# Kernel tuning notes

Hardware: AMD Instinct MI355X
Metric: run time of the kernel (lower is better)

The kernel has to match this reference:

```python
import jax, jax.numpy as jnp
import numpy as np

BITS = 50

def _xor(a, b):
    # binary XOR on {0,1} floats: a + b - 2ab
    return a + b - 2.0 * a * b

def _maj(a, b, c):
    # majority (carry-out of a full adder) on {0,1} floats
    return a * b + a * c + b * c - 2.0 * a * b * c

def setup_inputs() -> dict:
    key = jax.random.key(0)
    kA, kB = jax.random.split(key)
    N = 1_000_000
    A = jax.random.randint(kA, (N, BITS), 0, 2).astype(jnp.float32)
    B = jax.random.randint(kB, (N, BITS), 0, 2).astype(jnp.float32)
    return {"A": A, "B": B}

def reference(A, B):
    """A - B via two's complement ripple-carry: A + NOT(B) + 1, LSB first.
    Returns (result [..., 50], borrow [..., 1])."""
    not_b = 1.0 - B                      # VecNOT
    # scan over the 50 bits (sequential carry dependency)
    a_bits = jnp.moveaxis(A, -1, 0)      # [50, N]
    b_bits = jnp.moveaxis(not_b, -1, 0)  # [50, N]
    c0 = jnp.ones(A.shape[:-1], dtype=A.dtype)  # initial carry = 1

    def step(c, ab):
        a, b = ab
        s = _xor(_xor(a, b), c)          # FullAdder sum
        c_next = _maj(a, b, c)           # FullAdder carry
        return c_next, s

    c_final, sums = jax.lax.scan(step, c0, (a_bits, b_bits))
    result = jnp.moveaxis(sums, 0, -1)   # [N, 50]
    borrow = (1.0 - c_final)[..., None]  # borrow_not(carry), [N, 1]
    return result, borrow
```

## Files before the change

kernel.cpp:

```cpp
#include <hip/hip_runtime.h>


constexpr int BITS = 50;
constexpr unsigned long long MASK50 = (1ULL << BITS) - 1ULL;

__device__ inline unsigned long long shfl64(unsigned long long v, int src) {
    int lo = __shfl((int)(unsigned)(v & 0xffffffffULL), src, 64);
    int hi = __shfl((int)(unsigned)(v >> 32), src, 64);
    return ((unsigned long long)(unsigned)hi << 32) | (unsigned long long)(unsigned)lo;
}

__device__ inline unsigned long long spread2(unsigned long long x) {
    x = (x | (x << 16)) & 0x0000FFFF0000FFFFULL;
    x = (x | (x << 8))  & 0x00FF00FF00FF00FFULL;
    x = (x | (x << 4))  & 0x0F0F0F0F0F0F0F0FULL;
    x = (x | (x << 2))  & 0x3333333333333333ULL;
    x = (x | (x << 1))  & 0x5555555555555555ULL;
    return x;
}

__global__ __launch_bounds__(256) void Subtractor50Bit_kernel(
    const float* __restrict__ A, const float* __restrict__ B,
    float* __restrict__ out, int N)
{
    const int lane = threadIdx.x & 63;
    const int wv   = threadIdx.x >> 6;
    const long long waveIdx = (long long)blockIdx.x * 4 + wv;
    const long long rowBase = waveIdx * 64;
    if (rowBase >= N) return;

    if (rowBase + 64 <= N) {
        const long long eBase = rowBase * BITS;
        const float2* pa = (const float2*)(A + eBase) + lane;
        const float2* pb = (const float2*)(B + eBase) + lane;

        float2 fa[25], fb[25];
        #pragma unroll
        for (int t = 0; t < 25; ++t) fa[t] = pa[t * 64];
        #pragma unroll
        for (int t = 0; t < 25; ++t) fb[t] = pb[t * 64];

        __builtin_amdgcn_sched_barrier(0);

        unsigned long long wa = 0, wb = 0;
        const int  lane31 = lane & 31;
        const bool isLo   = lane < 32;
        #pragma unroll
        for (int t = 0; t < 25; ++t) {
            unsigned long long aE = __ballot(fa[t].x != 0.0f);
            unsigned long long aO = __ballot(fa[t].y != 0.0f);
            unsigned long long bE = __ballot(fb[t].x != 0.0f);
            unsigned long long bO = __ballot(fb[t].y != 0.0f);
            if (lane31 == t) {
                wa = isLo ? aE : aO;
                wb = isLo ? bE : bO;
            }
        }

        const int p0 = 25 * lane;
        const int w0 = p0 >> 6;
        const int sh = p0 & 63;

        unsigned long long aE0 = shfl64(wa, w0);
        unsigned long long aE1 = shfl64(wa, w0 + 1);
        unsigned long long aO0 = shfl64(wa, 32 + w0);
        unsigned long long aO1 = shfl64(wa, 33 + w0);
        unsigned long long bE0 = shfl64(wb, w0);
        unsigned long long bE1 = shfl64(wb, w0 + 1);
        unsigned long long bO0 = shfl64(wb, 32 + w0);
        unsigned long long bO1 = shfl64(wb, 33 + w0);

        unsigned long long evA = aE0 >> sh, odA = aO0 >> sh;
        unsigned long long evB = bE0 >> sh, odB = bO0 >> sh;
        if (sh > 39) {
            const int c = 64 - sh;
            evA |= aE1 << c; odA |= aO1 << c;
            evB |= bE1 << c; odB |= bO1 << c;
        }
        const unsigned long long M25 = (1ULL << 25) - 1ULL;
        evA &= M25; odA &= M25; evB &= M25; odB &= M25;

        unsigned long long av = spread2(evA) | (spread2(odA) << 1);
        unsigned long long bv = spread2(evB) | (spread2(odB) << 1);

        unsigned long long diff = (av - bv) & MASK50;
        float borrow = (av < bv) ? 1.0f : 0.0f;

        unsigned long long* po = (unsigned long long*)(out + eBase);
        #pragma unroll
        for (int j = 0; j < 25; ++j) {
            int q = j * 64 + lane;
            int r = q / 25;
            int k = 2 * (q - r * 25);
            unsigned long long dr = shfl64(diff, r);
            unsigned long long t2 = dr >> k;
            po[q] = ((t2 & 1ULL) ? 0x000000003F800000ULL : 0ULL)
                  | ((t2 & 2ULL) ? 0x3F80000000000000ULL : 0ULL);
        }
        out[(long long)N * BITS + rowBase + lane] = borrow;
    } else {
        long long r = rowBase + lane;
        if (r < N) {
            unsigned long long av = 0, bv = 0;
            for (int k = 0; k < BITS; ++k) {
                av |= (unsigned long long)(A[r * BITS + k] != 0.0f) << k;
                bv |= (unsigned long long)(B[r * BITS + k] != 0.0f) << k;
            }
            unsigned long long diff = (av - bv) & MASK50;
            for (int k = 0; k < BITS; ++k)
                out[r * BITS + k] = (float)((diff >> k) & 1ULL);
            out[(long long)N * BITS + r] = (av < bv) ? 1.0f : 0.0f;
        }
    }
}

extern "C" void kernel_launch(void* const* d_in, const int* in_sizes, int n_in,
                              void* d_out, int out_size, void* d_ws, size_t ws_size,
                              hipStream_t stream) {
    const float* A = (const float*)d_in[0];
    const float* B = (const float*)d_in[1];
    float* out = (float*)d_out;
    const int N = in_sizes[0] / BITS;

    const int waves  = (N + 63) / 64;
    const int blocks = (waves + 3) / 4;
    Subtractor50Bit_kernel<<<blocks, 256, 0, stream>>>(A, B, out, N);
}
```

Measured before the change: 447.8 us.

## Switch to grid-stride persistent waves and interleave loads with ballots

Replaces the one-wave-per-64-row-tile launch with a grid capped at 2048 blocks whose waves loop over tiles in grid-stride fashion, and adds an occupancy hint to launch bounds. The upfront loading of all 50 float2 values into registers, separated by a schedule barrier, is replaced by loading each pair inside the ballot loop. This cuts register pressure and block-launch overhead, but risks less memory-level parallelism per wave because loads are no longer all issued before the ballots. The tail rows are now handled by a single wave of block 0.

New measurement: 522.1 us. 16.6% more time.

```diff
diff --git a/kernel.cpp b/kernel.cpp
--- a/kernel.cpp
+++ b/kernel.cpp
@@ -19,38 +19,34 @@
     return x;
 }
 
-__global__ __launch_bounds__(256) void Subtractor50Bit_kernel(
+__global__ __launch_bounds__(256, 8) void Subtractor50Bit_kernel(
     const float* __restrict__ A, const float* __restrict__ B,
     float* __restrict__ out, int N)
 {
-    const int lane = threadIdx.x & 63;
-    const int wv   = threadIdx.x >> 6;
-    const long long waveIdx = (long long)blockIdx.x * 4 + wv;
-    const long long rowBase = waveIdx * 64;
-    if (rowBase >= N) return;
+    const int lane   = threadIdx.x & 63;
+    const int wv     = threadIdx.x >> 6;
+    const int lane31 = lane & 31;
+    const bool isLo  = lane < 32;
 
-    if (rowBase + 64 <= N) {
-        const long long eBase = rowBase * BITS;
+    const long long nTiles     = (long long)N >> 6;
+    const long long wavesTotal = (long long)gridDim.x * 4;
+
+    for (long long tile = (long long)blockIdx.x * 4 + wv;
+         tile < nTiles; tile += wavesTotal) {
+
+        const long long eBase = tile * 64 * BITS;
         const float2* pa = (const float2*)(A + eBase) + lane;
         const float2* pb = (const float2*)(B + eBase) + lane;
 
-        float2 fa[25], fb[25];
-        #pragma unroll
-        for (int t = 0; t < 25; ++t) fa[t] = pa[t * 64];
-        #pragma unroll
-        for (int t = 0; t < 25; ++t) fb[t] = pb[t * 64];
-
-        __builtin_amdgcn_sched_barrier(0);
-
         unsigned long long wa = 0, wb = 0;
-        const int  lane31 = lane & 31;
-        const bool isLo   = lane < 32;
         #pragma unroll
         for (int t = 0; t < 25; ++t) {
-            unsigned long long aE = __ballot(fa[t].x != 0.0f);
-            unsigned long long aO = __ballot(fa[t].y != 0.0f);
-            unsigned long long bE = __ballot(fb[t].x != 0.0f);
-            unsigned long long bO = __ballot(fb[t].y != 0.0f);
+            float2 va = pa[t * 64];
+            float2 vb = pb[t * 64];
+            unsigned long long aE = __ballot(va.x != 0.0f);
+            unsigned long long aO = __ballot(va.y != 0.0f);
+            unsigned long long bE = __ballot(vb.x != 0.0f);
+            unsigned long long bO = __ballot(vb.y != 0.0f);
             if (lane31 == t) {
                 wa = isLo ? aE : aO;
                 wb = isLo ? bE : bO;
@@ -97,9 +93,11 @@
             po[q] = ((t2 & 1ULL) ? 0x000000003F800000ULL : 0ULL)
                   | ((t2 & 2ULL) ? 0x3F80000000000000ULL : 0ULL);
         }
-        out[(long long)N * BITS + rowBase + lane] = borrow;
-    } else {
-        long long r = rowBase + lane;
+        out[(long long)N * BITS + tile * 64 + lane] = borrow;
+    }
+
+    if (blockIdx.x == 0 && wv == 0) {
+        long long r = nTiles * 64 + lane;
         if (r < N) {
             unsigned long long av = 0, bv = 0;
             for (int k = 0; k < BITS; ++k) {
@@ -122,7 +120,9 @@
     float* out = (float*)d_out;
     const int N = in_sizes[0] / BITS;
 
-    const int waves  = (N + 63) / 64;
-    const int blocks = (waves + 3) / 4;
-    Subtractor50Bit_kernel<<<blocks, 256, 0, stream>>>(A, B, out, N);
+    const long long nTiles = (long long)N >> 6;
+    long long want = (nTiles + 3) / 4;
+    if (want > 2048) want = 2048;
+    if (want < 1) want = 1;
+    Subtractor50Bit_kernel<<<(int)want, 256, 0, stream>>>(A, B, out, N);
 }
```
